# Kernel optimization log

Hardware: AMD Instinct MI355X
Metric: run time of the kernel (lower is better)

## Reference

```python
import jax, jax.numpy as jnp
import numpy as np
from jax import lax

N = 512          # batch size
A = 64 * 3 * 3 + 1  # 577 minibatch-disc input features
B = 32           # out_features of minibatch disc
C = 16           # kernel dimension


def leaky_relu(x, slope=0.2):
    return jnp.where(x >= 0, x, slope * x)


def setup_inputs() -> dict:
    key = jax.random.key(0)
    ks = jax.random.split(key, 9)
    readout = jax.random.normal(ks[0], (N, 1, 9, 9), dtype=jnp.float32)
    energy = jax.random.uniform(ks[1], (N,), dtype=jnp.float32)
    conv1_w = jax.random.normal(ks[2], (32, 1, 4, 4), dtype=jnp.float32) * 0.1
    conv2_w = jax.random.normal(ks[3], (64, 32, 4, 4), dtype=jnp.float32) * 0.05
    T = jax.random.normal(ks[4], (A, B * C), dtype=jnp.float32)  # init.normal(0,1)
    W1 = jax.random.normal(ks[5], (32, A + B), dtype=jnp.float32) * 0.04
    b1 = jax.random.normal(ks[6], (32,), dtype=jnp.float32) * 0.01
    W2 = jax.random.normal(ks[7], (1, 32), dtype=jnp.float32) * 0.1
    b2 = jax.random.normal(ks[8], (1,), dtype=jnp.float32) * 0.01
    return {"readout": readout, "energy": energy, "conv1_w": conv1_w,
            "conv2_w": conv2_w, "T": T, "W1": W1, "b1": b1, "W2": W2, "b2": b2}


def _conv(x, w):
    return lax.conv_general_dilated(
        x, w, window_strides=(1, 1), padding='VALID',
        dimension_numbers=('NCHW', 'OIHW', 'NCHW'))


def reference(readout, energy, conv1_w, conv2_w, T, W1, b1, W2, b2):
    n = readout.shape[0]
    # conv stack: (n,1,9,9) -> (n,32,6,6) -> (n,64,3,3)
    h = leaky_relu(_conv(readout, conv1_w))
    h = leaky_relu(_conv(h, conv2_w))
    hidden = h.reshape(n, -1)  # (n, 576)
    reco_energy = readout.reshape(n, -1).sum(axis=1)
    energy_diff = jnp.abs(reco_energy - energy)[:, None]  # (n,1)
    f = jnp.concatenate([hidden, energy_diff], axis=1)  # (n, 577)
    # minibatch discrimination
    M = (f @ T).reshape(n, B, C)                     # (n,B,C)
    # L1 pairwise distances, summed over kernel dim C: (n,n,B)
    L1 = jnp.abs(M[None, :, :, :] - M[:, None, :, :]).sum(axis=3)
    o = jnp.exp(-L1).sum(axis=0)                     # (n,B)
    x = jnp.concatenate([f, o], axis=1)              # (n, 609)
    x = leaky_relu(x @ W1.T + b1)
    x = jax.nn.sigmoid(x @ W2.T + b2)
    return x.squeeze()
```

## Files before the change

kernel.cpp:

```cpp
#include <hip/hip_runtime.h>

#define LRELU(v) ((v) >= 0.f ? (v) : 0.2f*(v))

#define ROROW(P, RB) \
    const float P##0=ro[(RB)+0], P##1=ro[(RB)+1], P##2=ro[(RB)+2], \
        P##3=ro[(RB)+3], P##4=ro[(RB)+4], P##5=ro[(RB)+5], \
        P##6=ro[(RB)+6], P##7=ro[(RB)+7], P##8=ro[(RB)+8];

#define C1X(X0,X1,X2,X3) \
    (wa.x*A##X0 + wa.y*A##X1 + wa.z*A##X2 + wa.w*A##X3 \
   + wb.x*B##X0 + wb.y*B##X1 + wb.z*B##X2 + wb.w*B##X3 \
   + wc.x*C##X0 + wc.y*C##X1 + wc.z*C##X2 + wc.w*C##X3 \
   + wd.x*D##X0 + wd.y*D##X1 + wd.z*D##X2 + wd.w*D##X3)

#define E0 q0.x
#define E1 q0.y
#define E2 q0.z
#define E3 q0.w
#define E4 q1.x
#define E5 q1.y
#define E6 q1.z
#define E7 q1.w
#define E8 q2.x
#define E9 q2.y
#define E10 q2.z
#define E11 q2.w
#define E12 q3.x
#define E13 q3.y
#define E14 q3.z
#define E15 q3.w
#define E16 q4.x
#define E17 q4.y
#define E18 q4.z
#define E19 q4.w
#define E20 q5.x
#define E21 q5.y
#define E22 q5.z
#define E23 q5.w
#define E24 q6.x
#define E25 q6.y
#define E26 q6.z
#define E27 q6.w
#define E28 q7.x
#define E29 q7.y
#define E30 q7.z
#define E31 q7.w
#define E32 q8.x
#define E33 q8.y
#define E34 q8.z
#define E35 q8.w

#define AT(P, A, B, C, D) a##P += w.x*E##A + w.y*E##B + w.z*E##C + w.w*E##D;

#define LD1(RK, K, BASE) { const int fidx_ = t + (K)*256; \
    const int woc_ = fidx_ >> 5, q4_ = fidx_ & 31; \
    RK = ((const float4*)w2)[(oc0 + woc_)*128 + (BASE) + q4_]; }
#define LDALL(BASE) LD1(r0,0,BASE) LD1(r1,1,BASE) LD1(r2,2,BASE) LD1(r3,3,BASE)
#define ST1(RK, K) { const int fidx_ = t + (K)*256; \
    const int woc_ = fidx_ >> 5, q4_ = fidx_ & 31; \
    *((float4*)&w2s[woc_*128 + ((q4_*4) ^ ((woc_ & 7) << 2))]) = RK; }
#define STALL ST1(r0,0) ST1(r1,1) ST1(r2,2) ST1(r3,3)

__global__ __launch_bounds__(256) void convf_kernel(
    const float* __restrict__ readout, const float* __restrict__ energy,
    const float* __restrict__ w1, const float* __restrict__ w2,
    const float* __restrict__ W1, float* __restrict__ f_ws,
    float* __restrict__ W1T)
{
    const int bid = blockIdx.x;
    const int n   = bid >> 1;
    const int och = bid & 1;
    const int oc0 = och << 5;
    const int t = threadIdx.x;
    __shared__ float ro[81];
    __shared__ float h1[1152];
    __shared__ float w2s[4096];
    __shared__ float red[2304];

    if (t < 81) ro[t] = readout[n*81 + t];
    __syncthreads();

    if (och == 0 && t < 64) {
        float v = ro[t];
        if (t < 17) v += ro[t + 64];
        #pragma unroll
        for (int m = 32; m; m >>= 1) v += __shfl_down(v, m);
        if (t == 0) f_ws[n*577 + 576] = fabsf(v - energy[n]);
    }

    if (t < 192) {
        const int oc1 = t & 31, y = t >> 5;
        const float4* wp4 = (const float4*)&w1[oc1*16];
        const float4 wa = wp4[0], wb = wp4[1], wc = wp4[2], wd = wp4[3];
        const int rb0 = y*9;
        ROROW(A, rb0)
        ROROW(B, rb0+9)
        ROROW(C, rb0+18)
        ROROW(D, rb0+27)
        float* hp = &h1[oc1*36 + y*6];
        float v;
        v = C1X(0,1,2,3); hp[0] = LRELU(v);
        v = C1X(1,2,3,4); hp[1] = LRELU(v);
        v = C1X(2,3,4,5); hp[2] = LRELU(v);
        v = C1X(3,4,5,6); hp[3] = LRELU(v);
        v = C1X(4,5,6,7); hp[4] = LRELU(v);
        v = C1X(5,6,7,8); hp[5] = LRELU(v);
    }

    float4 r0, r1, r2, r3;
    LDALL(0)
    __syncthreads();

    const int ich = t >> 5, ocl = t & 31;
    float a0=0.f,a1=0.f,a2=0.f,a3=0.f,a4=0.f,a5=0.f,a6=0.f,a7=0.f,a8=0.f;
    const int wbase = ocl*128;
    const int wswz  = (ocl & 7) << 2;

    for (int chunk = 0; chunk < 4; chunk++) {
        STALL
        __syncthreads();
        if (chunk < 3) { LDALL((chunk+1)*32) }
        {
            const int icw = ich;
            const int ic  = chunk*8 + ich;
            const float4* hp = (const float4*)&h1[ic*36];
            float4 q0=hp[0], q1=hp[1], q2=hp[2], q3=hp[3], q4=hp[4],
                   q5=hp[5], q6=hp[6], q7=hp[7], q8=hp[8];
            { float4 w = *((const float4*)&w2s[wbase + ((icw*16 + 0) ^ wswz)]);
              AT(0, 0,1,2,3)    AT(1, 1,2,3,4)    AT(2, 2,3,4,5)
              AT(3, 6,7,8,9)    AT(4, 7,8,9,10)   AT(5, 8,9,10,11)
              AT(6, 12,13,14,15) AT(7, 13,14,15,16) AT(8, 14,15,16,17) }
            { float4 w = *((const float4*)&w2s[wbase + ((icw*16 + 4) ^ wswz)]);
              AT(0, 6,7,8,9)    AT(1, 7,8,9,10)   AT(2, 8,9,10,11)
              AT(3, 12,13,14,15) AT(4, 13,14,15,16) AT(5, 14,15,16,17)
              AT(6, 18,19,20,21) AT(7, 19,20,21,22) AT(8, 20,21,22,23) }
            { float4 w = *((const float4*)&w2s[wbase + ((icw*16 + 8) ^ wswz)]);
              AT(0, 12,13,14,15) AT(1, 13,14,15,16) AT(2, 14,15,16,17)
              AT(3, 18,19,20,21) AT(4, 19,20,21,22) AT(5, 20,21,22,23)
              AT(6, 24,25,26,27) AT(7, 25,26,27,28) AT(8, 26,27,28,29) }
            { float4 w = *((const float4*)&w2s[wbase + ((icw*16 + 12) ^ wswz)]);
              AT(0, 18,19,20,21) AT(1, 19,20,21,22) AT(2, 20,21,22,23)
              AT(3, 24,25,26,27) AT(4, 25,26,27,28) AT(5, 26,27,28,29)
              AT(6, 30,31,32,33) AT(7, 31,32,33,34) AT(8, 32,33,34,35) }
        }
        __syncthreads();
    }

    {
        float* rp = &red[t*9];
        rp[0]=a0; rp[1]=a1; rp[2]=a2; rp[3]=a3; rp[4]=a4;
        rp[5]=a5; rp[6]=a6; rp[7]=a7; rp[8]=a8;
    }
    __syncthreads();
    for (int idx = t; idx < 288; idx += 256) {
        const int o2 = idx / 9, pos = idx % 9;
        float v = 0.f;
        #pragma unroll
        for (int k = 0; k < 8; k++) v += red[k*288 + idx];
        f_ws[n*577 + (oc0 + o2)*9 + pos] = LRELU(v);
    }

    if (bid < 8) {
        for (int idx = t; idx < 2436; idx += 256) {
            const int g = bid*2436 + idx;
            const int u = g & 31, a = g >> 5;
            W1T[g] = W1[u*609 + a];
        }
    }
}

__global__ __launch_bounds__(1024) void mgemm_kernel(
    const float* __restrict__ F, const float* __restrict__ T,
    float* __restrict__ M)
{
    const int t = threadIdx.x;
    const int rb = blockIdx.x >> 3, cb = blockIdx.x & 7;
    const int col = cb*64 + (t & 63);
    const int w = __builtin_amdgcn_readfirstlane(t >> 6);
    const int k0 = w*36;
    const int k1 = (w == 15) ? 577 : (k0 + 36);
    const int r0 = rb*8;
    __shared__ float red[16*520];

    const float* fbase = F + r0*577;
    const float* Tc = T + col;
    float c0=0.f,c1=0.f,c2=0.f,c3=0.f,c4=0.f,c5=0.f,c6=0.f,c7=0.f;
    #pragma unroll 4
    for (int k = k0; k < k1; ++k) {
        const float tv = Tc[k*512];
        const float* fr = fbase + k;
        c0 += fr[0]*tv;    c1 += fr[577]*tv;  c2 += fr[1154]*tv; c3 += fr[1731]*tv;
        c4 += fr[2308]*tv; c5 += fr[2885]*tv; c6 += fr[3462]*tv; c7 += fr[4039]*tv;
    }
    {
        const int cl = t & 63;
        float* rp = &red[w*520];
        rp[  0 + cl] = c0;  rp[ 64 + cl] = c1;
        rp[128 + cl] = c2;  rp[192 + cl] = c3;
        rp[256 + cl] = c4;  rp[320 + cl] = c5;
        rp[384 + cl] = c6;  rp[448 + cl] = c7;
    }
    __syncthreads();
    if (t < 512) {
        float v = 0.f;
        #pragma unroll
        for (int ks = 0; ks < 16; ks++) v += red[ks*520 + t];
        M[(r0 + (t >> 6))*512 + cb*64 + (t & 63)] = v;
    }
}

#define LDM(R0, R1, R2, R3, JOFF) { \
    const float4* p_ = (const float4*)&M[(j0+jl+(JOFF))*512 + b*16]; \
    R0 = p_[0]; R1 = p_[1]; R2 = p_[2]; R3 = p_[3]; }

#define S16(P0, P1, P2, P3) \
  (fabsf(v0.x-P0.x)+fabsf(v0.y-P0.y)+fabsf(v0.z-P0.z)+fabsf(v0.w-P0.w) \
  +fabsf(v1.x-P1.x)+fabsf(v1.y-P1.y)+fabsf(v1.z-P1.z)+fabsf(v1.w-P1.w) \
  +fabsf(v2.x-P2.x)+fabsf(v2.y-P2.y)+fabsf(v2.z-P2.z)+fabsf(v2.w-P2.w) \
  +fabsf(v3.x-P3.x)+fabsf(v3.y-P3.y)+fabsf(v3.z-P3.z)+fabsf(v3.w-P3.w))

__global__ __launch_bounds__(256) void pairwise_kernel(
    const float* __restrict__ M, float* __restrict__ o_part)
{
    const int jt  = blockIdx.x >> 5;
    const int isp = blockIdx.x & 31;
    const int t = threadIdx.x;
    const int b = t & 31, jl = t >> 5;
    const int j0 = jt * 32;
    __shared__ float mi[16*572];

    float4 mA0,mA1,mA2,mA3, mB0,mB1,mB2,mB3, mC0,mC1,mC2,mC3, mD0,mD1,mD2,mD3;
    LDM(mA0,mA1,mA2,mA3, 0)
    LDM(mB0,mB1,mB2,mB3, 8)
    LDM(mC0,mC1,mC2,mC3, 16)
    LDM(mD0,mD1,mD2,mD3, 24)

    const int i0 = isp * 16;
    #pragma unroll
    for (int k = 0; k < 8; k++) {
        const int q = k*256 + t;
        const int r = q >> 7;
        const int x = (q & 127) * 4;
        float4 v = *(const float4*)&M[(i0+r)*512 + x];
        *(float4*)&mi[r*572 + x + ((x>>5)<<2)] = v;
    }
    __syncthreads();

    float acc0 = 0.f, acc1 = 0.f, acc2 = 0.f, acc3 = 0.f;
    const int lbase = b*16 + ((b>>1)<<2);

    #pragma unroll 4
    for (int r = 0; r < 16; r++) {
        const float4* q_ = (const float4*)&mi[r*572 + lbase];
        const float4 v0 = q_[0], v1 = q_[1], v2 = q_[2], v3 = q_[3];
        acc0 += __expf(-(S16(mA0,mA1,mA2,mA3)));
        acc1 += __expf(-(S16(mB0,mB1,mB2,mB3)));
        acc2 += __expf(-(S16(mC0,mC1,mC2,mC3)));
        acc3 += __expf(-(S16(mD0,mD1,mD2,mD3)));
    }
    const int ob = isp*16384 + b;
    o_part[ob + (j0+jl   )*32] = acc0;
    o_part[ob + (j0+jl+8 )*32] = acc1;
    o_part[ob + (j0+jl+16)*32] = acc2;
    o_part[ob + (j0+jl+24)*32] = acc3;
}

__global__ __launch_bounds__(256) void mlp_kernel(
    const float* __restrict__ f, const float* __restrict__ o_part,
    const float* __restrict__ W1T, const float* __restrict__ b1v,
    const float* __restrict__ W2, const float* __restrict__ b2v,
    float* __restrict__ out)
{
    const int j = blockIdx.x;
    const int t = threadIdx.x;
    __shared__ float xs[609];
    __shared__ float red[256];

    for (int a = t; a < 577; a += 256) xs[a] = f[j*577 + a];
    {
        const int bb = t & 31, g = t >> 5;
        float ov = 0.f;
        #pragma unroll
        for (int k = 0; k < 4; k++)
            ov += o_part[(g + 8*k)*16384 + j*32 + bb];
        red[t] = ov;
    }
    __syncthreads();
    if (t < 32) {
        float ov = 0.f;
        #pragma unroll
        for (int g = 0; g < 8; g++) ov += red[t + g*32];
        xs[577 + t] = ov;
    }
    __syncthreads();

    const int u = t & 31, seg = t >> 5;
    float p = 0.f;
    #pragma unroll 4
    for (int a = seg; a < 609; a += 8)
        p += xs[a] * W1T[a*32 + u];
    red[t] = p;
    __syncthreads();

    if (t < 32) {
        float hid = red[t];
        #pragma unroll
        for (int s = 1; s < 8; s++) hid += red[t + s*32];
        hid += b1v[t];
        hid = LRELU(hid);
        float pr = hid * W2[t];
        #pragma unroll
        for (int mk = 16; mk; mk >>= 1) pr += __shfl_xor(pr, mk);
        if (t == 0) out[j] = 1.f / (1.f + __expf(-(pr + b2v[0])));
    }
}

extern "C" void kernel_launch(void* const* d_in, const int* in_sizes, int n_in,
                              void* d_out, int out_size, void* d_ws, size_t ws_size,
                              hipStream_t stream) {
    const float* readout = (const float*)d_in[0];
    const float* energy  = (const float*)d_in[1];
    const float* w1      = (const float*)d_in[2];
    const float* w2      = (const float*)d_in[3];
    const float* Tm      = (const float*)d_in[4];
    const float* W1      = (const float*)d_in[5];
    const float* b1v     = (const float*)d_in[6];
    const float* W2      = (const float*)d_in[7];
    const float* b2v     = (const float*)d_in[8];
    float* out = (float*)d_out;

    char* ws = (char*)d_ws;
    float* f_ws   = (float*)(ws);
    float* M_ws   = (float*)(ws + 512*577*4);
    float* o_ws   = (float*)(ws + 512*577*4 + 512*512*4);
    float* W1T_ws = (float*)(ws + 512*577*4 + 512*512*4 + 32*512*32*4);

    convf_kernel   <<<1024, 256, 0, stream>>>(readout, energy, w1, w2, W1, f_ws, W1T_ws);
    mgemm_kernel   <<<512, 1024, 0, stream>>>(f_ws, Tm, M_ws);
    pairwise_kernel<<<512, 256, 0, stream>>>(M_ws, o_ws);
    mlp_kernel     <<<512, 256, 0, stream>>>(f_ws, o_ws, W1T_ws, b1v, W2, b2v, out);
}
```

Measured before the change: 53.64 us.

## Fuse four stage kernels into one cooperative persistent kernel with grid syncs

Replaces the four separate launches (conv, M gemm, pairwise L1/exp, MLP) with a single cooperative kernel of 256 blocks x 1024 threads that runs each stage and separates them with grid.sync(). Each block now handles two samples per stage, and conv2 reads weights straight from global memory with a shuffle reduction instead of the staged shared-memory weight tiles. The aim is to remove launch overhead and inter-kernel gaps. In exchange it adds grid-wide barrier cost and lower parallelism per stage with only 256 blocks. The old four-kernel path is kept as a fallback if the cooperative launch fails.

```diff
diff --git a/kernel.cpp b/kernel.cpp
--- a/kernel.cpp
+++ b/kernel.cpp
@@ -1,11 +1,14 @@
 #include <hip/hip_runtime.h>
+#include <hip/hip_cooperative_groups.h>
+
+namespace cg = cooperative_groups;
 
 #define LRELU(v) ((v) >= 0.f ? (v) : 0.2f*(v))
 
 #define ROROW(P, RB) \
-    const float P##0=ro[(RB)+0], P##1=ro[(RB)+1], P##2=ro[(RB)+2], \
-        P##3=ro[(RB)+3], P##4=ro[(RB)+4], P##5=ro[(RB)+5], \
-        P##6=ro[(RB)+6], P##7=ro[(RB)+7], P##8=ro[(RB)+8];
+    const float P##0=rp[(RB)+0], P##1=rp[(RB)+1], P##2=rp[(RB)+2], \
+        P##3=rp[(RB)+3], P##4=rp[(RB)+4], P##5=rp[(RB)+5], \
+        P##6=rp[(RB)+6], P##7=rp[(RB)+7], P##8=rp[(RB)+8];
 
 #define C1X(X0,X1,X2,X3) \
     (wa.x*A##X0 + wa.y*A##X1 + wa.z*A##X2 + wa.w*A##X3 \
@@ -52,14 +55,244 @@
 
 #define AT(P, A, B, C, D) a##P += w.x*E##A + w.y*E##B + w.z*E##C + w.w*E##D;
 
-#define LD1(RK, K, BASE) { const int fidx_ = t + (K)*256; \
-    const int woc_ = fidx_ >> 5, q4_ = fidx_ & 31; \
-    RK = ((const float4*)w2)[(oc0 + woc_)*128 + (BASE) + q4_]; }
-#define LDALL(BASE) LD1(r0,0,BASE) LD1(r1,1,BASE) LD1(r2,2,BASE) LD1(r3,3,BASE)
-#define ST1(RK, K) { const int fidx_ = t + (K)*256; \
-    const int woc_ = fidx_ >> 5, q4_ = fidx_ & 31; \
-    *((float4*)&w2s[woc_*128 + ((q4_*4) ^ ((woc_ & 7) << 2))]) = RK; }
-#define STALL ST1(r0,0) ST1(r1,1) ST1(r2,2) ST1(r3,3)
+#define KYA0 { AT(0, 0,1,2,3)    AT(1, 1,2,3,4)    AT(2, 2,3,4,5) \
+               AT(3, 6,7,8,9)    AT(4, 7,8,9,10)   AT(5, 8,9,10,11) \
+               AT(6, 12,13,14,15) AT(7, 13,14,15,16) AT(8, 14,15,16,17) }
+#define KYA1 { AT(0, 6,7,8,9)    AT(1, 7,8,9,10)   AT(2, 8,9,10,11) \
+               AT(3, 12,13,14,15) AT(4, 13,14,15,16) AT(5, 14,15,16,17) \
+               AT(6, 18,19,20,21) AT(7, 19,20,21,22) AT(8, 20,21,22,23) }
+#define KYA2 { AT(0, 12,13,14,15) AT(1, 13,14,15,16) AT(2, 14,15,16,17) \
+               AT(3, 18,19,20,21) AT(4, 19,20,21,22) AT(5, 20,21,22,23) \
+               AT(6, 24,25,26,27) AT(7, 25,26,27,28) AT(8, 26,27,28,29) }
+#define KYA3 { AT(0, 18,19,20,21) AT(1, 19,20,21,22) AT(2, 20,21,22,23) \
+               AT(3, 24,25,26,27) AT(4, 25,26,27,28) AT(5, 26,27,28,29) \
+               AT(6, 30,31,32,33) AT(7, 31,32,33,34) AT(8, 32,33,34,35) }
+
+#define RED9A(M) \
+    a0+=__shfl_xor(a0,M); a1+=__shfl_xor(a1,M); a2+=__shfl_xor(a2,M); \
+    a3+=__shfl_xor(a3,M); a4+=__shfl_xor(a4,M); a5+=__shfl_xor(a5,M); \
+    a6+=__shfl_xor(a6,M); a7+=__shfl_xor(a7,M); a8+=__shfl_xor(a8,M);
+
+#define S16(P0, P1, P2, P3) \
+  (fabsf(v0.x-P0.x)+fabsf(v0.y-P0.y)+fabsf(v0.z-P0.z)+fabsf(v0.w-P0.w) \
+  +fabsf(v1.x-P1.x)+fabsf(v1.y-P1.y)+fabsf(v1.z-P1.z)+fabsf(v1.w-P1.w) \
+  +fabsf(v2.x-P2.x)+fabsf(v2.y-P2.y)+fabsf(v2.z-P2.z)+fabsf(v2.w-P2.w) \
+  +fabsf(v3.x-P3.x)+fabsf(v3.y-P3.y)+fabsf(v3.z-P3.z)+fabsf(v3.w-P3.w))
+
+__global__ __launch_bounds__(1024) void fused_kernel(
+    const float* __restrict__ readout, const float* __restrict__ energy,
+    const float* __restrict__ w1, const float* __restrict__ w2,
+    const float* __restrict__ Tm, const float* __restrict__ W1,
+    const float* __restrict__ b1v, const float* __restrict__ W2,
+    const float* __restrict__ b2v,
+    float* __restrict__ f_ws, float* __restrict__ Mw,
+    float* __restrict__ o_part, float* __restrict__ W1T,
+    float* __restrict__ out)
+{
+    __shared__ float smem[9152];
+    const int bid = blockIdx.x;
+    const int t = threadIdx.x;
+    cg::grid_group grid = cg::this_grid();
+
+    {
+        float* ro = smem;
+        float* h1 = smem + 192;
+
+        if (t < 162) {
+            const int sA = t / 81, i = t - sA*81;
+            ro[sA*96 + i] = readout[bid*162 + t];
+        }
+        __syncthreads();
+
+        if (t < 128) {
+            const int es = t >> 6, l = t & 63;
+            float v = ro[es*96 + l];
+            if (l < 17) v += ro[es*96 + l + 64];
+            #pragma unroll
+            for (int m = 32; m; m >>= 1) v += __shfl_down(v, m);
+            if (l == 0) f_ws[(2*bid+es)*577 + 576] = fabsf(v - energy[2*bid+es]);
+        }
+
+        if (t < 384) {
+            const int sA = (t >= 192) ? 1 : 0;
+            const int rem = t - sA*192;
+            const int oc1 = rem & 31, y = rem >> 5;
+            const float* rp = ro + sA*96;
+            const float4* wp4 = (const float4*)&w1[oc1*16];
+            const float4 wa = wp4[0], wb = wp4[1], wc = wp4[2], wd = wp4[3];
+            const int rb0 = y*9;
+            ROROW(A, rb0)
+            ROROW(B, rb0+9)
+            ROROW(C, rb0+18)
+            ROROW(D, rb0+27)
+            float* hp = &h1[sA*1152 + oc1*36 + y*6];
+            float v;
+            v = C1X(0,1,2,3); hp[0] = LRELU(v);
+            v = C1X(1,2,3,4); hp[1] = LRELU(v);
+            v = C1X(2,3,4,5); hp[2] = LRELU(v);
+            v = C1X(3,4,5,6); hp[3] = LRELU(v);
+            v = C1X(4,5,6,7); hp[4] = LRELU(v);
+            v = C1X(5,6,7,8); hp[5] = LRELU(v);
+        }
+        __syncthreads();
+
+        const int s2 = t >> 9, lt = t & 511;
+        const int oc = lt >> 3, ich = lt & 7;
+        float a0=0.f,a1=0.f,a2=0.f,a3=0.f,a4=0.f,a5=0.f,a6=0.f,a7=0.f,a8=0.f;
+        const float* hb = h1 + s2*1152;
+        #pragma unroll 1
+        for (int k = 0; k < 4; k++) {
+            const int ic = ich + k*8;
+            const float4* hp = (const float4*)&hb[ic*36];
+            const float4 q0=hp[0], q1=hp[1], q2=hp[2], q3=hp[3], q4=hp[4],
+                         q5=hp[5], q6=hp[6], q7=hp[7], q8=hp[8];
+            const float4* wpa = (const float4*)&w2[oc*512 + ic*16];
+            { float4 w = wpa[0]; KYA0 }
+            { float4 w = wpa[1]; KYA1 }
+            { float4 w = wpa[2]; KYA2 }
+            { float4 w = wpa[3]; KYA3 }
+        }
+        RED9A(1) RED9A(2) RED9A(4)
+
+        if (ich == 0) {
+            const int n = 2*bid + s2;
+            float* fa = &f_ws[n*577 + oc*9];
+            float v;
+            v=a0; fa[0]=LRELU(v); v=a1; fa[1]=LRELU(v); v=a2; fa[2]=LRELU(v);
+            v=a3; fa[3]=LRELU(v); v=a4; fa[4]=LRELU(v); v=a5; fa[5]=LRELU(v);
+            v=a6; fa[6]=LRELU(v); v=a7; fa[7]=LRELU(v); v=a8; fa[8]=LRELU(v);
+        }
+
+        if (bid < 8) {
+            for (int idx = t; idx < 2436; idx += 1024) {
+                const int g = bid*2436 + idx;
+                const int u = g & 31, a = g >> 5;
+                W1T[g] = W1[u*609 + a];
+            }
+        }
+    }
+    grid.sync();
+
+    {
+        float* redB = smem;
+        #pragma unroll 1
+        for (int it = 0; it < 2; it++) {
+            const int tt = bid*2 + it;
+            const int rb = tt >> 3, cb = tt & 7;
+            const int col = cb*64 + (t & 63);
+            const int w = __builtin_amdgcn_readfirstlane(t >> 6);
+            const int k0 = w*36;
+            const int k1 = (w == 15) ? 577 : (k0 + 36);
+            const int r0 = rb*8;
+            const float* fbase = f_ws + r0*577;
+            const float* Tc = Tm + col;
+            float c0=0.f,c1=0.f,c2=0.f,c3=0.f,c4=0.f,c5=0.f,c6=0.f,c7=0.f;
+            #pragma unroll 4
+            for (int k = k0; k < k1; ++k) {
+                const float tv = Tc[k*512];
+                const float* fr = fbase + k;
+                c0 += fr[0]*tv;    c1 += fr[577]*tv;  c2 += fr[1154]*tv; c3 += fr[1731]*tv;
+                c4 += fr[2308]*tv; c5 += fr[2885]*tv; c6 += fr[3462]*tv; c7 += fr[4039]*tv;
+            }
+            {
+                const int cl = t & 63;
+                float* rp = &redB[w*520];
+                rp[  0 + cl] = c0;  rp[ 64 + cl] = c1;
+                rp[128 + cl] = c2;  rp[192 + cl] = c3;
+                rp[256 + cl] = c4;  rp[320 + cl] = c5;
+                rp[384 + cl] = c6;  rp[448 + cl] = c7;
+            }
+            __syncthreads();
+            if (t < 512) {
+                float v = 0.f;
+                #pragma unroll
+                for (int ks = 0; ks < 16; ks++) v += redB[ks*520 + t];
+                Mw[(r0 + (t >> 6))*512 + cb*64 + (t & 63)] = v;
+            }
+            __syncthreads();
+        }
+    }
+    grid.sync();
+
+    {
+        float* mi = smem;
+        const int b = t & 31, jl = (t >> 5) & 31;
+        #pragma unroll 1
+        for (int u = 0; u < 2; u++) {
+            const int unit = bid*2 + u;
+            const int jt = unit >> 5, isp = unit & 31;
+            const int j0 = jt*32, i0 = isp*16;
+
+            float4 mA0,mA1,mA2,mA3;
+            { const float4* p_ = (const float4*)&Mw[(j0+jl)*512 + b*16];
+              mA0=p_[0]; mA1=p_[1]; mA2=p_[2]; mA3=p_[3]; }
+
+            #pragma unroll
+            for (int k = 0; k < 2; k++) {
+                const int q = k*1024 + t;
+                const int r = q >> 7;
+                const int x = (q & 127) * 4;
+                float4 v = *(const float4*)&Mw[(i0+r)*512 + x];
+                *(float4*)&mi[r*572 + x + ((x>>5)<<2)] = v;
+            }
+            __syncthreads();
+
+            float acc = 0.f;
+            const int lbase = b*16 + ((b>>1)<<2);
+            #pragma unroll 4
+            for (int r = 0; r < 16; r++) {
+                const float4* q_ = (const float4*)&mi[r*572 + lbase];
+                const float4 v0 = q_[0], v1 = q_[1], v2 = q_[2], v3 = q_[3];
+                acc += __expf(-(S16(mA0,mA1,mA2,mA3)));
+            }
+            o_part[isp*16384 + (j0+jl)*32 + b] = acc;
+            __syncthreads();
+        }
+    }
+    grid.sync();
+
+    {
+        const int s2 = t >> 9, lt = t & 511;
+        const int j = 2*bid + s2;
+        float* xs   = smem + s2*640;
+        float* redD = smem + 1280 + s2*512;
+        const int u = lt & 31, g = lt >> 5;
+
+        for (int a = lt; a < 577; a += 512) xs[a] = f_ws[j*577 + a];
+        {
+            float ov = o_part[g*16384 + j*32 + u]
+                     + o_part[(g+16)*16384 + j*32 + u];
+            redD[lt] = ov;
+        }
+        __syncthreads();
+        if (lt < 32) {
+            float ov = 0.f;
+            #pragma unroll
+            for (int gg = 0; gg < 16; gg++) ov += redD[lt + gg*32];
+            xs[577 + lt] = ov;
+        }
+        __syncthreads();
+
+        float p = 0.f;
+        #pragma unroll 4
+        for (int a = g; a < 609; a += 16)
+            p += xs[a] * W1T[a*32 + u];
+        redD[lt] = p;
+        __syncthreads();
+
+        if (lt < 32) {
+            float hid = 0.f;
+            #pragma unroll
+            for (int s = 0; s < 16; s++) hid += redD[lt + s*32];
+            hid += b1v[lt];
+            hid = LRELU(hid);
+            float pr = hid * W2[lt];
+            #pragma unroll
+            for (int mk = 16; mk; mk >>= 1) pr += __shfl_xor(pr, mk);
+            if (lt == 0) out[j] = 1.f / (1.f + __expf(-(pr + b2v[0])));
+        }
+    }
+}
 
 __global__ __launch_bounds__(256) void convf_kernel(
     const float* __restrict__ readout, const float* __restrict__ energy,
@@ -90,6 +323,7 @@
 
     if (t < 192) {
         const int oc1 = t & 31, y = t >> 5;
+        const float* rp = ro;
         const float4* wp4 = (const float4*)&w1[oc1*16];
         const float4 wa = wp4[0], wb = wp4[1], wc = wp4[2], wd = wp4[3];
         const int rb0 = y*9;
@@ -108,7 +342,14 @@
     }
 
     float4 r0, r1, r2, r3;
-    LDALL(0)
+    { const int fidx_ = t;            const int woc_ = fidx_ >> 5, q4_ = fidx_ & 31;
+      r0 = ((const float4*)w2)[(oc0 + woc_)*128 + q4_]; }
+    { const int fidx_ = t + 256;      const int woc_ = fidx_ >> 5, q4_ = fidx_ & 31;
+      r1 = ((const float4*)w2)[(oc0 + woc_)*128 + q4_]; }
+    { const int fidx_ = t + 512;      const int woc_ = fidx_ >> 5, q4_ = fidx_ & 31;
+      r2 = ((const float4*)w2)[(oc0 + woc_)*128 + q4_]; }
+    { const int fidx_ = t + 768;      const int woc_ = fidx_ >> 5, q4_ = fidx_ & 31;
+      r3 = ((const float4*)w2)[(oc0 + woc_)*128 + q4_]; }
     __syncthreads();
 
     const int ich = t >> 5, ocl = t & 31;
@@ -117,31 +358,36 @@
     const int wswz  = (ocl & 7) << 2;
 
     for (int chunk = 0; chunk < 4; chunk++) {
-        STALL
-        __syncthreads();
-        if (chunk < 3) { LDALL((chunk+1)*32) }
+        { const int fidx_ = t;       const int woc_ = fidx_ >> 5, q4_ = fidx_ & 31;
+          *((float4*)&w2s[woc_*128 + ((q4_*4) ^ ((woc_ & 7) << 2))]) = r0; }
+        { const int fidx_ = t + 256; const int woc_ = fidx_ >> 5, q4_ = fidx_ & 31;
+          *((float4*)&w2s[woc_*128 + ((q4_*4) ^ ((woc_ & 7) << 2))]) = r1; }
+        { const int fidx_ = t + 512; const int woc_ = fidx_ >> 5, q4_ = fidx_ & 31;
+          *((float4*)&w2s[woc_*128 + ((q4_*4) ^ ((woc_ & 7) << 2))]) = r2; }
+        { const int fidx_ = t + 768; const int woc_ = fidx_ >> 5, q4_ = fidx_ & 31;
+          *((float4*)&w2s[woc_*128 + ((q4_*4) ^ ((woc_ & 7) << 2))]) = r3; }
+        __syncthreads();
+        if (chunk < 3) {
+            const int base = (chunk+1)*32;
+            { const int fidx_ = t;       const int woc_ = fidx_ >> 5, q4_ = fidx_ & 31;
+              r0 = ((const float4*)w2)[(oc0 + woc_)*128 + base + q4_]; }
+            { const int fidx_ = t + 256; const int woc_ = fidx_ >> 5, q4_ = fidx_ & 31;
+              r1 = ((const float4*)w2)[(oc0 + woc_)*128 + base + q4_]; }
+            { const int fidx_ = t + 512; const int woc_ = fidx_ >> 5, q4_ = fidx_ & 31;
+              r2 = ((const float4*)w2)[(oc0 + woc_)*128 + base + q4_]; }
+            { const int fidx_ = t + 768; const int woc_ = fidx_ >> 5, q4_ = fidx_ & 31;
+              r3 = ((const float4*)w2)[(oc0 + woc_)*128 + base + q4_]; }
+        }
         {
             const int icw = ich;
             const int ic  = chunk*8 + ich;
             const float4* hp = (const float4*)&h1[ic*36];
             float4 q0=hp[0], q1=hp[1], q2=hp[2], q3=hp[3], q4=hp[4],
                    q5=hp[5], q6=hp[6], q7=hp[7], q8=hp[8];
-            { float4 w = *((const float4*)&w2s[wbase + ((icw*16 + 0) ^ wswz)]);
-              AT(0, 0,1,2,3)    AT(1, 1,2,3,4)    AT(2, 2,3,4,5)
-              AT(3, 6,7,8,9)    AT(4, 7,8,9,10)   AT(5, 8,9,10,11)
-              AT(6, 12,13,14,15) AT(7, 13,14,15,16) AT(8, 14,15,16,17) }
-            { float4 w = *((const float4*)&w2s[wbase + ((icw*16 + 4) ^ wswz)]);
-              AT(0, 6,7,8,9)    AT(1, 7,8,9,10)   AT(2, 8,9,10,11)
-              AT(3, 12,13,14,15) AT(4, 13,14,15,16) AT(5, 14,15,16,17)
-              AT(6, 18,19,20,21) AT(7, 19,20,21,22) AT(8, 20,21,22,23) }
-            { float4 w = *((const float4*)&w2s[wbase + ((icw*16 + 8) ^ wswz)]);
-              AT(0, 12,13,14,15) AT(1, 13,14,15,16) AT(2, 14,15,16,17)
-              AT(3, 18,19,20,21) AT(4, 19,20,21,22) AT(5, 20,21,22,23)
-              AT(6, 24,25,26,27) AT(7, 25,26,27,28) AT(8, 26,27,28,29) }
-            { float4 w = *((const float4*)&w2s[wbase + ((icw*16 + 12) ^ wswz)]);
-              AT(0, 18,19,20,21) AT(1, 19,20,21,22) AT(2, 20,21,22,23)
-              AT(3, 24,25,26,27) AT(4, 25,26,27,28) AT(5, 26,27,28,29)
-              AT(6, 30,31,32,33) AT(7, 31,32,33,34) AT(8, 32,33,34,35) }
+            { float4 w = *((const float4*)&w2s[wbase + ((icw*16 + 0) ^ wswz)]);  KYA0 }
+            { float4 w = *((const float4*)&w2s[wbase + ((icw*16 + 4) ^ wswz)]);  KYA1 }
+            { float4 w = *((const float4*)&w2s[wbase + ((icw*16 + 8) ^ wswz)]);  KYA2 }
+            { float4 w = *((const float4*)&w2s[wbase + ((icw*16 + 12) ^ wswz)]); KYA3 }
         }
         __syncthreads();
     }
@@ -212,12 +458,6 @@
 #define LDM(R0, R1, R2, R3, JOFF) { \
     const float4* p_ = (const float4*)&M[(j0+jl+(JOFF))*512 + b*16]; \
     R0 = p_[0]; R1 = p_[1]; R2 = p_[2]; R3 = p_[3]; }
-
-#define S16(P0, P1, P2, P3) \
-  (fabsf(v0.x-P0.x)+fabsf(v0.y-P0.y)+fabsf(v0.z-P0.z)+fabsf(v0.w-P0.w) \
-  +fabsf(v1.x-P1.x)+fabsf(v1.y-P1.y)+fabsf(v1.z-P1.z)+fabsf(v1.w-P1.w) \
-  +fabsf(v2.x-P2.x)+fabsf(v2.y-P2.y)+fabsf(v2.z-P2.z)+fabsf(v2.w-P2.w) \
-  +fabsf(v3.x-P3.x)+fabsf(v3.y-P3.y)+fabsf(v3.z-P3.z)+fabsf(v3.w-P3.w))
 
 __global__ __launch_bounds__(256) void pairwise_kernel(
     const float* __restrict__ M, float* __restrict__ o_part)
@@ -335,8 +575,17 @@
     float* o_ws   = (float*)(ws + 512*577*4 + 512*512*4);
     float* W1T_ws = (float*)(ws + 512*577*4 + 512*512*4 + 32*512*32*4);
 
-    convf_kernel   <<<1024, 256, 0, stream>>>(readout, energy, w1, w2, W1, f_ws, W1T_ws);
-    mgemm_kernel   <<<512, 1024, 0, stream>>>(f_ws, Tm, M_ws);
-    pairwise_kernel<<<512, 256, 0, stream>>>(M_ws, o_ws);
-    mlp_kernel     <<<512, 256, 0, stream>>>(f_ws, o_ws, W1T_ws, b1v, W2, b2v, out);
+    void* args[] = {
+        (void*)&readout, (void*)&energy, (void*)&w1, (void*)&w2, (void*)&Tm,
+        (void*)&W1, (void*)&b1v, (void*)&W2, (void*)&b2v,
+        (void*)&f_ws, (void*)&M_ws, (void*)&o_ws, (void*)&W1T_ws, (void*)&out
+    };
+    hipError_t err = hipLaunchCooperativeKernel((void*)fused_kernel, dim3(256),
+                                                dim3(1024), args, 0, stream);
+    if (err != hipSuccess) {
+        convf_kernel   <<<1024, 256, 0, stream>>>(readout, energy, w1, w2, W1, f_ws, W1T_ws);
+        mgemm_kernel   <<<512, 1024, 0, stream>>>(f_ws, Tm, M_ws);
+        pairwise_kernel<<<512, 256, 0, stream>>>(M_ws, o_ws);
+        mlp_kernel     <<<512, 256, 0, stream>>>(f_ws, o_ws, W1T_ws, b1v, W2, b2v, out);
+    }
 }
```

Result: slower. 149.5 us (+178.7%).
